# Kernel optimization log

Hardware: AMD Instinct MI355X
Metric: run time of the kernel (lower is better)

## Reference

```python
import jax, jax.numpy as jnp
import numpy as np

N_HEADS = 12
LN_EPS = 1e-5


def _layernorm(x, w):
    # torch F.layer_norm (no affine) then * w
    x = x.astype(jnp.float32)
    mu = jnp.mean(x, axis=-1, keepdims=True)
    var = jnp.mean(jnp.square(x - mu), axis=-1, keepdims=True)
    return (x - mu) * jax.lax.rsqrt(var + LN_EPS) * w


def _rotate_half(x):
    x1, x2 = jnp.split(x, 2, axis=-1)
    return jnp.concatenate([-x2, x1], axis=-1)


def setup_inputs() -> dict:
    key = jax.random.key(0)
    ks = jax.random.split(key, 10)
    b, s, dim, cond, hd = 2, 4096, 768, 768, 64
    mlp = 4 * dim
    # rotary tables
    inv_freq = 1.0 / (10000.0 ** (np.arange(0, hd, 2, dtype=np.float32) / hd))
    t = np.arange(s, dtype=np.float32)
    freqs = np.einsum('s,d->sd', t, inv_freq)           # [s, hd/2]
    emb = np.concatenate([freqs, freqs], axis=-1)        # [s, hd]
    cos = jnp.asarray(np.cos(emb))[None, :, None, None, :]
    sin = jnp.asarray(np.sin(emb))[None, :, None, None, :]
    sc = lambda f: 1.0 / np.sqrt(f)
    return {
        'x': jax.random.normal(ks[0], (b, s, dim), jnp.float32),
        'cos': cos,
        'sin': sin,
        'c': jax.random.normal(ks[1], (b, cond), jnp.float32),
        'attention_mask': jax.random.randint(ks[2], (b, s), 0, 2, jnp.int32),
        'ln1_w': jnp.ones((dim,), jnp.float32),
        'Wqkv': jax.random.normal(ks[3], (3 * dim, dim), jnp.float32) * sc(dim),
        'Wout': jax.random.normal(ks[4], (dim, dim), jnp.float32) * sc(dim),
        'ln2_w': jnp.ones((dim,), jnp.float32),
        'W1': jax.random.normal(ks[5], (mlp, dim), jnp.float32) * sc(dim),
        'b1': jnp.zeros((mlp,), jnp.float32),
        'W2': jax.random.normal(ks[6], (dim, mlp), jnp.float32) * sc(mlp),
        'b2': jnp.zeros((dim,), jnp.float32),
        'Wada': jax.random.normal(ks[7], (6 * dim, cond), jnp.float32) * 0.02,
        'bada': jnp.zeros((6 * dim,), jnp.float32),
    }


def reference(x, cos, sin, c, attention_mask, ln1_w, Wqkv, Wout, ln2_w, W1, b1, W2, b2, Wada, bada):
    b, s, dim = x.shape
    h, hd = N_HEADS, dim // N_HEADS
    # adaLN modulation: [b, 6*dim] -> six [b, 1, dim] chunks
    mod = (c @ Wada.T + bada)[:, None, :]
    shift_msa, scale_msa, gate_msa, shift_mlp, scale_mlp, gate_mlp = jnp.split(mod, 6, axis=2)

    x_skip = x
    hdn = _layernorm(x, ln1_w) * (1.0 + scale_msa) + shift_msa
    qkv = (hdn @ Wqkv.T).reshape(b, s, 3, h, hd)
    qkv = qkv * cos + _rotate_half(qkv) * sin            # RoPE on q, k, and v (as in source)
    q = jnp.transpose(qkv[:, :, 0], (0, 2, 1, 3))        # [b, h, s, hd]
    k = jnp.transpose(qkv[:, :, 1], (0, 2, 1, 3))
    v = jnp.transpose(qkv[:, :, 2], (0, 2, 1, 3))

    m = attention_mask.astype(bool)
    pair = m[:, None, :, None] & m[:, None, None, :]     # [b, 1, s, s]
    bias = jnp.where(pair, 0.0, -1e9).astype(q.dtype)

    scores = jnp.einsum('bhqd,bhkd->bhqk', q, k) / jnp.sqrt(jnp.asarray(hd, q.dtype))
    attn = jax.nn.softmax(scores + bias, axis=-1)
    o = jnp.einsum('bhqk,bhkd->bhqd', attn, v)
    o = jnp.transpose(o, (0, 2, 1, 3)).reshape(b, s, dim)

    # inference-mode bias_dropout_add_scale (dropout off)
    x = x_skip + gate_msa * (o @ Wout.T)
    h2 = _layernorm(x, ln2_w) * (1.0 + scale_mlp) + shift_mlp
    mlp = jax.nn.gelu(h2 @ W1.T + b1, approximate=True) @ W2.T + b2
    return x + gate_mlp * mlp
```

## Files before the change

kernel.cpp:

```cpp
#include <hip/hip_runtime.h>
#include <stdint.h>


typedef unsigned short u16;
typedef __attribute__((ext_vector_type(4))) float f32x4;
typedef __attribute__((ext_vector_type(8))) short short8;
typedef __attribute__((ext_vector_type(4))) short s16x4;
typedef __attribute__((ext_vector_type(8))) __bf16 bf16x8;

__device__ __forceinline__ float b2f(u16 u){
  union { unsigned int i; float f; } v; v.i = ((unsigned int)u) << 16; return v.f;
}
__device__ __forceinline__ u16 f2b(float f){
  union { float f; unsigned int i; } v; v.f = f;
  unsigned int u = v.i;
  u = u + 0x7FFFu + ((u >> 16) & 1u);
  return (u16)(u >> 16);
}
__device__ __forceinline__ f32x4 mfma16(short8 a, short8 b, f32x4 c){
  return __builtin_amdgcn_mfma_f32_16x16x32_bf16(
      __builtin_bit_cast(bf16x8, a), __builtin_bit_cast(bf16x8, b), c, 0, 0, 0);
}
__device__ __forceinline__ void gload16(const void* g, void* l){
  void* gnc = const_cast<void*>(g);
  __builtin_amdgcn_global_load_lds((__attribute__((address_space(1))) void*)gnc,
                                   (__attribute__((address_space(3))) void*)l, 16, 0, 0);
}

__global__ __launch_bounds__(256) void cvt4_k(
    const float* __restrict__ s0, u16* __restrict__ d0,
    const float* __restrict__ s1, u16* __restrict__ d1,
    const float* __restrict__ s2, u16* __restrict__ d2,
    const float* __restrict__ s3, u16* __restrict__ d3)
{
  int i = blockIdx.x*256 + threadIdx.x;
  const float* src; u16* dst; int j = i;
  if (j < 442368){ src = s0; dst = d0; }
  else if ((j -= 442368) < 147456){ src = s1; dst = d1; }
  else if ((j -= 147456) < 589824){ src = s2; dst = d2; }
  else { j -= 589824; src = s3; dst = d3; }
  float4 v = *(const float4*)(src + (size_t)j*4);
  s16x4 o; o[0]=(short)f2b(v.x); o[1]=(short)f2b(v.y);
  o[2]=(short)f2b(v.z); o[3]=(short)f2b(v.w);
  *(s16x4*)(dst + (size_t)j*4) = o;
}

__global__ __launch_bounds__(64) void scan_k(const int* __restrict__ mask,
    int* __restrict__ idx, int* __restrict__ nvalid, float* __restrict__ vm)
{
  int b = blockIdx.x, l = threadIdx.x;
  const int* m = mask + b*4096;
  int base = 0;
  for (int i0 = 0; i0 < 4096; i0 += 64){
    int v = m[i0 + l] != 0;
    unsigned long long bal = __ballot(v);
    int pre = __popcll(bal & ((1ull << l) - 1ull));
    if (v) idx[b*4096 + base + pre] = i0 + l;
    base += (int)__popcll(bal);
  }
  if (l == 0) nvalid[b] = base;
  if (b == 0) for (int i = l; i < 24*64; i += 64) vm[i] = 0.f;
}

__global__ __launch_bounds__(256) void mod_k(const float* __restrict__ c,
    const float* __restrict__ Wada, const float* __restrict__ bada, float* __restrict__ modb)
{
  int o = blockIdx.x*4 + (threadIdx.x >> 6);
  int l = threadIdx.x & 63;
  int b = o / 4608, j = o - b*4608;
  const float* cp = c + b*768;
  const float* wp = Wada + (size_t)j*768;
  float s = 0.f;
  for (int k = l; k < 768; k += 64) s += cp[k] * wp[k];
  #pragma unroll
  for (int d=1; d<64; d<<=1) s += __shfl_xor(s, d);
  if (l == 0) modb[o] = s + bada[j];
}

__global__ __launch_bounds__(256) void ln_mod_k(const float* __restrict__ xin,
    u16* __restrict__ out, const float* __restrict__ lnw, const float* __restrict__ modb,
    int shift_c, int scale_c)
{
  int row = blockIdx.x;
  int b = row >> 12;
  const float* xp = xin + (size_t)row*768;
  int t = threadIdx.x;
  float v[3]; float s = 0.f, s2 = 0.f;
  #pragma unroll
  for (int i=0;i<3;i++){ float f = xp[t + i*256]; v[i] = f; s += f; s2 += f*f; }
  #pragma unroll
  for (int d=1; d<64; d<<=1){ s += __shfl_xor(s, d); s2 += __shfl_xor(s2, d); }
  __shared__ float rs_[4], rs2_[4];
  int w = t >> 6;
  if ((t & 63) == 0){ rs_[w] = s; rs2_[w] = s2; }
  __syncthreads();
  s  = rs_[0]+rs_[1]+rs_[2]+rs_[3];
  s2 = rs2_[0]+rs2_[1]+rs2_[2]+rs2_[3];
  float mu  = s * (1.f/768.f);
  float var = fmaxf(s2 * (1.f/768.f) - mu*mu, 0.f);
  float rstd = rsqrtf(var + 1e-5f);
  const float* scp = modb + b*4608 + scale_c*768;
  const float* shp = modb + b*4608 + shift_c*768;
  #pragma unroll
  for (int i=0;i<3;i++){
    int d = t + i*256;
    float f = (v[i]-mu)*rstd*lnw[d];
    f = f*(1.f + scp[d]) + shp[d];
    out[(size_t)row*768 + d] = f2b(f);
  }
}

template<int EPI>
__global__ __launch_bounds__(256) void gemm_k(
    const u16* __restrict__ A, const u16* __restrict__ Bt, void* __restrict__ Cv,
    int M, int N, int K,
    const float* __restrict__ addend, const float* __restrict__ modb,
    const float* __restrict__ bias,
    const float* __restrict__ cosb, const float* __restrict__ sinb,
    u16* __restrict__ qO, u16* __restrict__ kO, u16* __restrict__ vO)
{
  __shared__ __align__(16) u16 As[128*64];
  __shared__ __align__(16) u16 Bs[128*64];
  const int bm = blockIdx.x, bn = blockIdx.y;
  const int tid = threadIdx.x;
  const int w = tid >> 6, l = tid & 63;
  const int wr = w >> 1, wc = w & 1;
  const int l15 = l & 15, lg = l >> 4;
  f32x4 acc[4][4] = {};

  for (int k0 = 0; k0 < K; k0 += 64){
    #pragma unroll
    for (int i=0;i<4;i++){
      int e = i*256 + tid;
      int r = e >> 3, ch = e & 7;
      int sc = ch ^ (r & 7);
      gload16(A  + (size_t)(bm*128 + r)*K + k0 + sc*8, &As[e*8]);
      gload16(Bt + (size_t)(bn*128 + r)*K + k0 + sc*8, &Bs[e*8]);
    }
    __syncthreads();
    #pragma unroll
    for (int kk=0;kk<2;kk++){
      short8 af[4], bfv[4];
      #pragma unroll
      for (int i=0;i<4;i++){
        int ra = wr*64 + i*16 + l15;
        af[i]  = *(const short8*)&As[ra*64 + (((kk*4)+lg) ^ (ra&7))*8];
        int rb = wc*64 + i*16 + l15;
        bfv[i] = *(const short8*)&Bs[rb*64 + (((kk*4)+lg) ^ (rb&7))*8];
      }
      #pragma unroll
      for (int m=0;m<4;m++)
        #pragma unroll
        for (int n=0;n<4;n++)
          acc[m][n] = mfma16(af[m], bfv[n], acc[m][n]);
    }
    __syncthreads();
  }

  if constexpr (EPI == 4){
    const int colseg = bn*128 + wc*64;
    const int qi = colseg / 768;
    const int h  = (colseg - qi*768) >> 6;
    const float qs = (qi == 0) ? 0.1803368801111601f : 1.f;
    u16* dst = (qi == 0) ? qO : (qi == 1) ? kO : vO;
    #pragma unroll
    for (int m=0;m<4;m++){
      #pragma unroll
      for (int r=0;r<4;r++){
        int row = bm*128 + wr*64 + m*16 + lg*4 + r;
        int s = row & 4095, bb = row >> 12;
        size_t obase = ((size_t)(bb*12 + h)*4096 + s)*64;
        #pragma unroll
        for (int n2=0;n2<2;n2++){
          int d1 = n2*16 + l15;
          int d2 = d1 + 32;
          float c1 = cosb[s*64 + d1], s1 = sinb[s*64 + d1];
          float c2 = cosb[s*64 + d2], s2 = sinb[s*64 + d2];
          float x1 = acc[m][n2][r], x2 = acc[m][n2+2][r];
          dst[obase + d1] = f2b((x1*c1 - x2*s1)*qs);
          dst[obase + d2] = f2b((x2*c2 + x1*s2)*qs);
        }
      }
    }
    return;
  }

  #pragma unroll
  for (int m=0;m<4;m++){
    int row0 = bm*128 + wr*64 + m*16 + lg*4;
    #pragma unroll
    for (int n=0;n<4;n++){
      int col = bn*128 + wc*64 + n*16 + l15;
      #pragma unroll
      for (int r=0;r<4;r++){
        int row = row0 + r;
        size_t idx = (size_t)row*N + col;
        float v = acc[m][n][r];
        if constexpr (EPI == 0){
          ((u16*)Cv)[idx] = f2b(v);
        } else if constexpr (EPI == 1){
          float g = modb[(row>>12)*4608 + 2*768 + col];
          ((float*)Cv)[idx] = addend[idx] + g*v;
        } else if constexpr (EPI == 2){
          float u = v + bias[col];
          float t0 = 0.7978845608028654f*(u + 0.044715f*u*u*u);
          ((u16*)Cv)[idx] = f2b(0.5f*u*(1.0f + tanhf(t0)));
        } else if constexpr (EPI == 3){
          float g = modb[(row>>12)*4608 + 5*768 + col];
          float u = v + bias[col];
          ((float*)Cv)[idx] = addend[idx] + g*u;
        }
      }
    }
  }
}

__global__ __launch_bounds__(256) void gath_k(const u16* __restrict__ kT,
    const u16* __restrict__ vS, const int* __restrict__ idx,
    const int* __restrict__ nvalid, u16* __restrict__ kc, u16* __restrict__ vTc)
{
  __shared__ __align__(16) u16 tile[64][72];
  int j0 = blockIdx.x*64, bh = blockIdx.y;
  int b = bh / 12;
  int nv = nvalid[b];
  int npad = (nv + 511) & ~511;
  if (j0 >= npad) return;
  int t = threadIdx.x;
  #pragma unroll
  for (int i=0;i<2;i++){
    int e = i*256 + t;
    int r = e >> 3, ch = e & 7;
    int j = j0 + r;
    short8 kv8 = {}, vv8 = {};
    if (j < nv){
      int src = idx[b*4096 + j];
      kv8 = *(const short8*)(kT + ((size_t)bh*4096 + src)*64 + ch*8);
      vv8 = *(const short8*)(vS + ((size_t)bh*4096 + src)*64 + ch*8);
    }
    *(short8*)(kc + ((size_t)bh*4096 + j)*64 + ch*8) = kv8;
    *(short8*)&tile[r][ch*8] = vv8;
  }
  __syncthreads();
  #pragma unroll
  for (int i=0;i<2;i++){
    int e = i*256 + t;
    int dd = e >> 3, s0 = (e & 7)*8;
    short8 ov;
    #pragma unroll
    for (int k2=0;k2<8;k2++) ov[k2] = (short)tile[s0+k2][dd];
    *(short8*)(vTc + ((size_t)bh*64 + dd)*4096 + j0 + s0) = ov;
  }
}

__global__ __launch_bounds__(256) void vmean2_k(const u16* __restrict__ vS,
                                                float* __restrict__ vm)
{
  int bh = blockIdx.y, r0 = blockIdx.x*256;
  int t = threadIdx.x, d = t & 63, g = t >> 6;
  const u16* p = vS + ((size_t)bh*4096 + r0)*64 + d;
  float s = 0.f;
  for (int k = g; k < 256; k += 4) s += b2f(p[(size_t)k*64]);
  __shared__ float red[4][64];
  red[g][d] = s; __syncthreads();
  if (g == 0) atomicAdd(&vm[bh*64 + d], red[0][d]+red[1][d]+red[2][d]+red[3][d]);
}

#define AT_BODY(KT, KQK, KST, VPV, VST, STC, STN)                              \
{                                                                              \
  { int k3 = (KT)+3 < bodies ? (KT)+3 : bodies-1;                              \
    gload16(kbase + (size_t)(k3*64+sr)*64 + ssc*8, &Ks[KST][tid*8]); }         \
  { int v2 = (KT)+2 < bodies ? (KT)+2 : bodies-1;                              \
    gload16(vbase + (size_t)sr*4096 + v2*64 + ssc*8, &Vs[VST][tid*8]); }       \
  asm volatile("s_waitcnt vmcnt(2)" ::: "memory");        \
  if ((KT)+1 < bodies){                                                        \
    __builtin_amdgcn_s_setprio(1);                                             \
    _Pragma("unroll")                                                          \
    for (int n=0;n<4;n++){                                                     \
      int R = n*16 + l15;                                                      \
      f32x4 a_ = {};                                                           \
      _Pragma("unroll")                                                        \
      for (int kk=0;kk<2;kk++){                                                \
        short8 ka = *(const short8*)&Ks[KQK][R*64 + (((kk<<2)+lg) ^ (R&7))*8]; \
        a_ = mfma16(ka, bq[kk], a_);                                           \
      }                                                                        \
      STN[n] = a_;                                                             \
    }                                                                          \
    __builtin_amdgcn_s_setprio(0);                                             \
  }                                                                            \
  const int base_ = kbase0 + (KT)*64;                                          \
  if (base_ < nv){                          \
    float p_[4][4]; float ts_ = 0.f;                                           \
    if (base_ + 64 <= nv){                      \
      _Pragma("unroll")                                                        \
      for (int n=0;n<4;n++)                                                    \
        _Pragma("unroll")                                                      \
        for (int r=0;r<4;r++){                                                 \
          float e_ = __builtin_amdgcn_exp2f(STC[n][r]);                        \
          p_[n][r] = e_; ts_ += e_;                                            \
        }                                                                      \
    } else {                                                \
      _Pragma("unroll")                                                        \
      for (int n=0;n<4;n++)                                                    \
        _Pragma("unroll")                                                      \
        for (int r=0;r<4;r++){                                                 \
          int ki_ = base_ + n*16 + lg*4 + r;                                   \
          float e_ = (ki_ < nv) ? __builtin_amdgcn_exp2f(STC[n][r]) : 0.f;     \
          p_[n][r] = e_; ts_ += e_;                                            \
        }                                                                      \
    }                                                                          \
    ts_ += __shfl_xor(ts_, 16);                                                \
    ts_ += __shfl_xor(ts_, 32);                                                \
    l_run += ts_;                                                              \
    _Pragma("unroll")                                                          \
    for (int n=0;n<4;n++){                                                     \
      unsigned p01_, p23_;                                                     \
      asm("v_cvt_pk_bf16_f32 %0, %1, %2" : "=v"(p01_) : "v"(p_[n][0]), "v"(p_[n][1])); \
      asm("v_cvt_pk_bf16_f32 %0, %1, %2" : "=v"(p23_) : "v"(p_[n][2]), "v"(p_[n][3])); \
      int s0_ = n*16 + lg*4;                                                   \
      int off_ = (((s0_>>3) ^ (l15&7))<<3) + (s0_&7);                          \
      *(unsigned*)&Ps[w][l15*64 + off_]     = p01_;                            \
      *(unsigned*)&Ps[w][l15*64 + off_ + 2] = p23_;                            \
    }                                                                          \
    __builtin_amdgcn_s_setprio(1);                                             \
    _Pragma("unroll")                                                          \
    for (int kk=0;kk<2;kk++){                                                  \
      int ch_ = (kk<<2) + lg;                                                  \
      short8 bp_ = *(const short8*)&Ps[w][l15*64 + ((ch_ ^ (l15&7))<<3)];      \
      _Pragma("unroll")                                                        \
      for (int n=0;n<4;n++){                                                   \
        int R = n*16 + l15;                                                    \
        short8 va_ = *(const short8*)&Vs[VPV][R*64 + ((ch_ ^ (R&7))<<3)];      \
        oacc[n] = mfma16(va_, bp_, oacc[n]);                                   \
      }                                                                        \
    }                                                                          \
    __builtin_amdgcn_s_setprio(0);                                             \
  }                                                                            \
  __builtin_amdgcn_s_barrier();                                                \
}

__global__ __launch_bounds__(512) void attn_k(
    const u16* __restrict__ qT, const u16* __restrict__ kc, const u16* __restrict__ vTc,
    const int* __restrict__ nvalid, float* __restrict__ po, float* __restrict__ pl)
{
  __shared__ __align__(16) u16 Ks[4][64*64];
  __shared__ __align__(16) u16 Vs[4][64*64];
  __shared__ __align__(16) u16 Ps[8][16*64];
  const int qt = blockIdx.x, bh = blockIdx.y, kv = blockIdx.z;
  const int b = bh / 12;
  const int tid = threadIdx.x, w = tid >> 6, l = tid & 63;
  const int l15 = l & 15, lg = l >> 4;
  const int nv = nvalid[b];
  const int bodies = ((nv + 511) & ~511) >> 7;
  const int k0 = kv * bodies;
  const int kbase0 = k0 * 64;

  short8 bq[2];
  {
    const u16* qp = qT + ((size_t)bh*4096 + qt*128 + w*16 + l15)*64 + lg*8;
    bq[0] = *(const short8*)qp;
    bq[1] = *(const short8*)(qp + 32);
  }
  const u16* kbase = kc + ((size_t)bh*4096 + (size_t)kbase0)*64;
  const u16* vbase = vTc + (size_t)bh*64*4096 + (size_t)kbase0;

  float l_run = 0.f;
  f32x4 oacc[4] = {};

  const int sr = tid >> 3, ssc = (tid & 7) ^ (sr & 7);

  gload16(kbase + (size_t)sr*64 + ssc*8,            &Ks[0][tid*8]);
  gload16(kbase + (size_t)(64+sr)*64 + ssc*8,       &Ks[1][tid*8]);
  gload16(kbase + (size_t)(128+sr)*64 + ssc*8,      &Ks[2][tid*8]);
  gload16(vbase + (size_t)sr*4096 + ssc*8,          &Vs[0][tid*8]);
  gload16(vbase + (size_t)sr*4096 + 64 + ssc*8,     &Vs[1][tid*8]);
  asm volatile("s_waitcnt vmcnt(0)" ::: "memory");
  __builtin_amdgcn_s_barrier();

  f32x4 stA[4], stB[4];
  #pragma unroll
  for (int n=0;n<4;n++){
    int R = n*16 + l15;
    f32x4 a_ = {};
    #pragma unroll
    for (int kk=0;kk<2;kk++){
      short8 ka = *(const short8*)&Ks[0][R*64 + (((kk<<2)+lg) ^ (R&7))*8];
      a_ = mfma16(ka, bq[kk], a_);
    }
    stA[n] = a_;
  }

  for (int kt = 0; kt < bodies; kt += 4){
    AT_BODY(kt+0, 1, 3, 0, 2, stA, stB)
    AT_BODY(kt+1, 2, 0, 1, 3, stB, stA)
    AT_BODY(kt+2, 3, 1, 2, 0, stA, stB)
    AT_BODY(kt+3, 0, 2, 3, 1, stB, stA)
  }

  const int qrow = qt*128 + w*16 + l15;
  float* pob = po + (((size_t)kv*24 + bh)*4096 + qrow)*64;
  #pragma unroll
  for (int n=0;n<4;n++)
    *(f32x4*)&pob[n*16 + lg*4] = oacc[n];
  if (lg == 0) pl[((size_t)kv*24 + bh)*4096 + qrow] = l_run;
}

__global__ __launch_bounds__(256) void comb_k(const float* __restrict__ po,
    const float* __restrict__ pl, const int* __restrict__ mask,
    const float* __restrict__ vm, u16* __restrict__ o)
{
  int row = blockIdx.x;
  int b = row >> 12, s = row & 4095;
  bool fq = mask[row] != 0;
  int t = threadIdx.x;
  #pragma unroll
  for (int i=0;i<3;i++){
    int j = t + i*256;
    int h = j >> 6, d = j & 63;
    size_t pi = (((size_t)b*12 + h)*4096 + s)*64 + d;
    size_t li = ((size_t)b*12 + h)*4096 + s;
    float O = po[pi] + po[(size_t)24*4096*64 + pi];
    float L = pl[li] + pl[(size_t)24*4096 + li];
    float v = fq ? O / L : vm[(b*12 + h)*64 + d]*(1.f/4096.f);
    o[(size_t)row*768 + j] = f2b(v);
  }
}

extern "C" void kernel_launch(void* const* d_in, const int* in_sizes, int n_in,
                              void* d_out, int out_size, void* d_ws, size_t ws_size,
                              hipStream_t stream)
{
  const float* x    = (const float*)d_in[0];
  const float* cosb = (const float*)d_in[1];
  const float* sinb = (const float*)d_in[2];
  const float* c    = (const float*)d_in[3];
  const int* amask  = (const int*)d_in[4];
  const float* ln1w = (const float*)d_in[5];
  const float* Wqkv = (const float*)d_in[6];
  const float* Wout = (const float*)d_in[7];
  const float* ln2w = (const float*)d_in[8];
  const float* W1   = (const float*)d_in[9];
  const float* b1   = (const float*)d_in[10];
  const float* W2   = (const float*)d_in[11];
  const float* b2   = (const float*)d_in[12];
  const float* Wada = (const float*)d_in[13];
  const float* bada = (const float*)d_in[14];

  char* ws = (char*)d_ws;
  size_t off = 0;
  auto take = [&](size_t bytes)->char*{
    char* p = ws + off; off = (off + bytes + 255) & ~(size_t)255; return p;
  };
  float* modb = (float*)take(9216*sizeof(float));
  float* vmean= (float*)take(24*64*sizeof(float));
  int*   idx  = (int*)take(8192*sizeof(int));
  int*   nvld = (int*)take(2*sizeof(int));
  u16* hdn  = (u16*)take((size_t)8192*768*2);
  u16* bufA = (u16*)take((size_t)8192*3072*2);
  u16* vS   = (u16*)take((size_t)8192*768*2);
  u16* qTb  = (u16*)take((size_t)8192*768*2);
  u16* kTb  = (u16*)take((size_t)8192*768*2);
  u16* kc   = (u16*)take((size_t)8192*768*2);
  u16* vTc  = (u16*)take((size_t)8192*768*2);
  u16* ob   = (u16*)take((size_t)8192*768*2);
  u16* WqkvB= (u16*)take((size_t)2304*768*2);
  u16* WoutB= (u16*)take((size_t)768*768*2);
  u16* W1B  = (u16*)take((size_t)3072*768*2);
  u16* W2B  = (u16*)take((size_t)768*3072*2);
  float* out = (float*)d_out;
  float* x1 = out;
  float* po = (float*)bufA;
  float* pl = (float*)hdn;

  cvt4_k<<<6912, 256, 0, stream>>>(Wqkv, WqkvB, Wout, WoutB, W1, W1B, W2, W2B);
  scan_k<<<2, 64, 0, stream>>>(amask, idx, nvld, vmean);

  mod_k  <<<2304, 256, 0, stream>>>(c, Wada, bada, modb);
  ln_mod_k<<<8192, 256, 0, stream>>>(x, hdn, ln1w, modb, 0, 1);
  gemm_k<4><<<dim3(64,18), 256, 0, stream>>>(hdn, WqkvB, nullptr, 8192, 2304, 768,
                                             nullptr, nullptr, nullptr,
                                             cosb, sinb, qTb, kTb, vS);
  gath_k <<<dim3(64,24), 256, 0, stream>>>(kTb, vS, idx, nvld, kc, vTc);
  vmean2_k<<<dim3(16,24), 256, 0, stream>>>(vS, vmean);
  attn_k <<<dim3(32,24,2), 512, 0, stream>>>(qTb, kc, vTc, nvld, po, pl);
  comb_k <<<8192, 256, 0, stream>>>(po, pl, amask, vmean, ob);
  gemm_k<1><<<dim3(64,6), 256, 0, stream>>>(ob, WoutB, x1, 8192, 768, 768,
                                            x, modb, nullptr,
                                            nullptr, nullptr, nullptr, nullptr, nullptr);
  ln_mod_k<<<8192, 256, 0, stream>>>(x1, hdn, ln2w, modb, 3, 4);
  gemm_k<2><<<dim3(64,24), 256, 0, stream>>>(hdn, W1B, bufA, 8192, 3072, 768,
                                             nullptr, nullptr, b1,
                                             nullptr, nullptr, nullptr, nullptr, nullptr);
  gemm_k<3><<<dim3(64,6), 256, 0, stream>>>(bufA, W2B, out, 8192, 768, 3072,
                                            x1, modb, b2,
                                            nullptr, nullptr, nullptr, nullptr, nullptr);
}
```

Measured before the change: 356.9 us.

## Trim dead KV tiles, defer row-sum reduction, store partial outputs in bf16

The attention kernel now caps its loop at the number of 64-key tiles that actually contain valid keys for its KV split, rounded up to the unroll of 4, instead of always running all bodies. The per-tile cross-lane shuffle reduction of the softmax denominator is moved out of the loop and done once at the end. Partial output accumulators are written as bf16 rather than fp32, halving the split-combine traffic read by comb_k. Rounding partial sums to bf16 before combining adds extra precision loss.

Result: no change. 358.1 us (+0.3%).

```diff
diff --git a/kernel.cpp b/kernel.cpp
--- a/kernel.cpp
+++ b/kernel.cpp
@@ -267,12 +267,12 @@
 
 #define AT_BODY(KT, KQK, KST, VPV, VST, STC, STN)                              \
 {                                                                              \
-  { int k3 = (KT)+3 < bodies ? (KT)+3 : bodies-1;                              \
+  { int k3 = (KT)+3 < brun ? (KT)+3 : brun-1;                                  \
     gload16(kbase + (size_t)(k3*64+sr)*64 + ssc*8, &Ks[KST][tid*8]); }         \
-  { int v2 = (KT)+2 < bodies ? (KT)+2 : bodies-1;                              \
+  { int v2 = (KT)+2 < brun ? (KT)+2 : brun-1;                                  \
     gload16(vbase + (size_t)sr*4096 + v2*64 + ssc*8, &Vs[VST][tid*8]); }       \
   asm volatile("s_waitcnt vmcnt(2)" ::: "memory");        \
-  if ((KT)+1 < bodies){                                                        \
+  if ((KT)+1 < brun){                                                          \
     __builtin_amdgcn_s_setprio(1);                                             \
     _Pragma("unroll")                                                          \
     for (int n=0;n<4;n++){                                                     \
@@ -289,14 +289,14 @@
   }                                                                            \
   const int base_ = kbase0 + (KT)*64;                                          \
   if (base_ < nv){                          \
-    float p_[4][4]; float ts_ = 0.f;                                           \
+    float p_[4][4];                                                            \
     if (base_ + 64 <= nv){                      \
       _Pragma("unroll")                                                        \
       for (int n=0;n<4;n++)                                                    \
         _Pragma("unroll")                                                      \
         for (int r=0;r<4;r++){                                                 \
           float e_ = __builtin_amdgcn_exp2f(STC[n][r]);                        \
-          p_[n][r] = e_; ts_ += e_;                                            \
+          p_[n][r] = e_; l_run += e_;                                          \
         }                                                                      \
     } else {                                                \
       _Pragma("unroll")                                                        \
@@ -305,12 +305,9 @@
         for (int r=0;r<4;r++){                                                 \
           int ki_ = base_ + n*16 + lg*4 + r;                                   \
           float e_ = (ki_ < nv) ? __builtin_amdgcn_exp2f(STC[n][r]) : 0.f;     \
-          p_[n][r] = e_; ts_ += e_;                                            \
+          p_[n][r] = e_; l_run += e_;                                          \
         }                                                                      \
     }                                                                          \
-    ts_ += __shfl_xor(ts_, 16);                                                \
-    ts_ += __shfl_xor(ts_, 32);                                                \
-    l_run += ts_;                                                              \
     _Pragma("unroll")                                                          \
     for (int n=0;n<4;n++){                                                     \
       unsigned p01_, p23_;                                                     \
@@ -340,7 +337,7 @@
 
 __global__ __launch_bounds__(512) void attn_k(
     const u16* __restrict__ qT, const u16* __restrict__ kc, const u16* __restrict__ vTc,
-    const int* __restrict__ nvalid, float* __restrict__ po, float* __restrict__ pl)
+    const int* __restrict__ nvalid, u16* __restrict__ po, float* __restrict__ pl)
 {
   __shared__ __align__(16) u16 Ks[4][64*64];
   __shared__ __align__(16) u16 Vs[4][64*64];
@@ -353,6 +350,8 @@
   const int bodies = ((nv + 511) & ~511) >> 7;
   const int k0 = kv * bodies;
   const int kbase0 = k0 * 64;
+  const int nb_live = (nv - kbase0 + 63) >> 6;
+  const int brun = min(bodies, (nb_live + 3) & ~3);
 
   short8 bq[2];
   {
@@ -389,22 +388,29 @@
     stA[n] = a_;
   }
 
-  for (int kt = 0; kt < bodies; kt += 4){
+  for (int kt = 0; kt < brun; kt += 4){
     AT_BODY(kt+0, 1, 3, 0, 2, stA, stB)
     AT_BODY(kt+1, 2, 0, 1, 3, stB, stA)
     AT_BODY(kt+2, 3, 1, 2, 0, stA, stB)
     AT_BODY(kt+3, 0, 2, 3, 1, stB, stA)
   }
 
+  l_run += __shfl_xor(l_run, 16);
+  l_run += __shfl_xor(l_run, 32);
+
   const int qrow = qt*128 + w*16 + l15;
-  float* pob = po + (((size_t)kv*24 + bh)*4096 + qrow)*64;
-  #pragma unroll
-  for (int n=0;n<4;n++)
-    *(f32x4*)&pob[n*16 + lg*4] = oacc[n];
+  u16* pob = po + (((size_t)kv*24 + bh)*4096 + qrow)*64;
+  #pragma unroll
+  for (int n=0;n<4;n++){
+    unsigned q01 = (unsigned)f2b(oacc[n][0]) | ((unsigned)f2b(oacc[n][1]) << 16);
+    unsigned q23 = (unsigned)f2b(oacc[n][2]) | ((unsigned)f2b(oacc[n][3]) << 16);
+    *(unsigned*)&pob[n*16 + lg*4]     = q01;
+    *(unsigned*)&pob[n*16 + lg*4 + 2] = q23;
+  }
   if (lg == 0) pl[((size_t)kv*24 + bh)*4096 + qrow] = l_run;
 }
 
-__global__ __launch_bounds__(256) void comb_k(const float* __restrict__ po,
+__global__ __launch_bounds__(256) void comb_k(const u16* __restrict__ po,
     const float* __restrict__ pl, const int* __restrict__ mask,
     const float* __restrict__ vm, u16* __restrict__ o)
 {
@@ -418,7 +424,7 @@
     int h = j >> 6, d = j & 63;
     size_t pi = (((size_t)b*12 + h)*4096 + s)*64 + d;
     size_t li = ((size_t)b*12 + h)*4096 + s;
-    float O = po[pi] + po[(size_t)24*4096*64 + pi];
+    float O = b2f(po[pi]) + b2f(po[(size_t)24*4096*64 + pi]);
     float L = pl[li] + pl[(size_t)24*4096 + li];
     float v = fq ? O / L : vm[(b*12 + h)*64 + d]*(1.f/4096.f);
     o[(size_t)row*768 + j] = f2b(v);
@@ -468,7 +474,7 @@
   u16* W2B  = (u16*)take((size_t)768*3072*2);
   float* out = (float*)d_out;
   float* x1 = out;
-  float* po = (float*)bufA;
+  u16*   po = (u16*)bufA;
   float* pl = (float*)hdn;
 
   cvt4_k<<<6912, 256, 0, stream>>>(Wqkv, WqkvB, Wout, WoutB, W1, W1B, W2, W2B);
```
